# Optimization experiments

Measured on AMD Instinct MI355X. Metric: run time of the kernel, lower is better.

## Reference

```python
import jax, jax.numpy as jnp
import numpy as np

N_NODES = 50000
N_EDGES = 800000
IN_CH = 512
HID = 256
HEADS = 8
OUT_CH = 64


def _glorot(key, shape):
    fan_in = shape[0] if len(shape) == 2 else shape[-1]
    return jax.random.normal(key, shape, jnp.float32) / jnp.sqrt(jnp.float32(fan_in))


def setup_inputs() -> dict:
    key = jax.random.key(0)
    ks = jax.random.split(key, 16)
    C = HID // HEADS  # 32, per-head dim
    return {
        "x": jax.random.normal(ks[0], (N_NODES, IN_CH), jnp.float32),
        "edge_index": jax.random.randint(ks[1], (2, N_EDGES), 0, N_NODES, jnp.int32),
        # layer 0: in -> heads*C, concat
        "W0": _glorot(ks[2], (IN_CH, HEADS * C)),
        "a_src0": _glorot(ks[3], (HEADS, C)),
        "a_dst0": _glorot(ks[4], (HEADS, C)),
        "b0": jnp.zeros((HEADS * C,), jnp.float32),
        # layer 1: hidden -> heads*C, concat
        "W1": _glorot(ks[5], (HID, HEADS * C)),
        "a_src1": _glorot(ks[6], (HEADS, C)),
        "a_dst1": _glorot(ks[7], (HEADS, C)),
        "b1": jnp.zeros((HEADS * C,), jnp.float32),
        # layer 2: hidden -> out_ch, 1 head, mean (concat=False)
        "W2": _glorot(ks[8], (HID, 1 * OUT_CH)),
        "a_src2": _glorot(ks[9], (1, OUT_CH)),
        "a_dst2": _glorot(ks[10], (1, OUT_CH)),
        "b2": jnp.zeros((OUT_CH,), jnp.float32),
    }


def gat_conv(x, W, a_src, a_dst, b, src, dst, concat):
    """PyG GATConv (self-loops already appended to src/dst), eval mode."""
    N = x.shape[0]
    H, C = a_src.shape
    h = (x @ W).reshape(N, H, C)                      # [N,H,C]
    alpha_src = jnp.sum(h * a_src, axis=-1)           # [N,H]
    alpha_dst = jnp.sum(h * a_dst, axis=-1)           # [N,H]
    e = jax.nn.leaky_relu(alpha_src[src] + alpha_dst[dst], 0.2)  # [E,H]
    # softmax over incoming edges per destination node
    m = jax.ops.segment_max(e, dst, num_segments=N)   # [N,H]
    m = jnp.where(jnp.isfinite(m), m, 0.0)
    w = jnp.exp(e - m[dst])
    s = jax.ops.segment_sum(w, dst, num_segments=N)
    alpha = w / (s[dst] + 1e-16)                      # [E,H]
    out = jax.ops.segment_sum(alpha[:, :, None] * h[src], dst, num_segments=N)
    out = out.reshape(N, H * C) if concat else out.mean(axis=1)
    return out + b


def reference(x, edge_index, W0, a_src0, a_dst0, b0, W1, a_src1, a_dst1, b1, W2, a_src2, a_dst2, b2):
    N = x.shape[0]
    loop = jnp.arange(N, dtype=edge_index.dtype)      # add_self_loops=True
    src = jnp.concatenate([edge_index[0], loop])
    dst = jnp.concatenate([edge_index[1], loop])
    # dropout is identity in eval mode
    h = jax.nn.elu(gat_conv(x, W0, a_src0, a_dst0, b0, src, dst, True))
    h = jax.nn.elu(gat_conv(h, W1, a_src1, a_dst1, b1, src, dst, True))
    h = gat_conv(h, W2, a_src2, a_dst2, b2, src, dst, False)
    return jax.nn.log_softmax(h, axis=1)
```

## Files before the change

kernel.cpp:

```cpp
#include <hip/hip_runtime.h>
#include <hip/hip_bf16.h>

typedef __attribute__((ext_vector_type(8))) short short8;
typedef __attribute__((ext_vector_type(4))) float f32x4;
typedef __attribute__((ext_vector_type(2))) float f32x2;
typedef __attribute__((ext_vector_type(4))) unsigned short us4;

__device__ __forceinline__ ushort f2bf(float f) {
    unsigned u = __float_as_uint(f);
    u += 0x7FFFu + ((u >> 16) & 1u);
    return (ushort)(u >> 16);
}
__device__ __forceinline__ float bf2f(ushort h) {
    return __uint_as_float(((unsigned)h) << 16);
}
__device__ __forceinline__ float lrelu(float e) { return (e >= 0.f) ? e : 0.2f * e; }
__device__ __forceinline__ unsigned char f2fp8(float v) {
    return (unsigned char)(__builtin_amdgcn_cvt_pk_fp8_f32(v, v, 0, false) & 0xFF);
}
__device__ __forceinline__ void gload16(const void* g, void* l) {
    __builtin_amdgcn_global_load_lds(
        (const __attribute__((address_space(1))) unsigned int*)g,
        (__attribute__((address_space(3))) unsigned int*)l, 16, 0, 0);
}
__device__ __forceinline__ short8 cvt8(f32x4 a, f32x4 b) {
    short8 v;
#pragma unroll
    for (int j = 0; j < 4; ++j) {
        v[j] = (short)f2bf(a[j]);
        v[4 + j] = (short)f2bf(b[j]);
    }
    return v;
}

__global__ void k_hist(const int* __restrict__ dst, int* __restrict__ deg, int e) {
    int i = blockIdx.x * blockDim.x + threadIdx.x;
    if (i < e) atomicAdd(&deg[dst[i]], 1);
}
__global__ void k_scanA(const int* __restrict__ deg, int* __restrict__ bsum, int n) {
    __shared__ int sd[256];
    int t = blockIdx.x * 256 + threadIdx.x;
    sd[threadIdx.x] = (t < n) ? deg[t] + 1 : 0;
    __syncthreads();
    for (int off = 128; off > 0; off >>= 1) {
        if (threadIdx.x < off) sd[threadIdx.x] += sd[threadIdx.x + off];
        __syncthreads();
    }
    if (threadIdx.x == 0) bsum[blockIdx.x] = sd[0];
}
__global__ void k_scanC(const int* __restrict__ deg, const int* __restrict__ bsum,
                        int* __restrict__ rowptr, int* __restrict__ cursor,
                        int n, int etot, int nb) {
    __shared__ int sb[256];
    __shared__ int sd[256];
    __shared__ int sbx[256];
    int i = threadIdx.x;
    int bv = (i < nb) ? bsum[i] : 0;
    sb[i] = bv;
    __syncthreads();
    for (int off = 1; off < 256; off <<= 1) {
        int tv = (i >= off) ? sb[i - off] : 0;
        __syncthreads();
        sb[i] += tv;
        __syncthreads();
    }
    sbx[i] = sb[i] - bv;
    __syncthreads();
    int boff = sbx[blockIdx.x];

    int t = blockIdx.x * 256 + i;
    int v = (t < n) ? deg[t] + 1 : 0;
    sd[i] = v;
    __syncthreads();
    for (int off = 1; off < 256; off <<= 1) {
        int tv = (i >= off) ? sd[i - off] : 0;
        __syncthreads();
        sd[i] += tv;
        __syncthreads();
    }
    if (t < n) {
        int ex = boff + sd[i] - v;
        rowptr[t] = ex;
        cursor[t] = ex;
        if (t == n - 1) rowptr[n] = etot;
    }
}
__global__ void k_scatter(const int* __restrict__ ei, int* __restrict__ cursor,
                          int* __restrict__ col, int e, int n) {
    int i = blockIdx.x * blockDim.x + threadIdx.x;
    int etot = e + n;
    if (i >= etot) return;
    int s, d;
    if (i < e) { s = ei[i]; d = ei[e + i]; }
    else       { s = i - e; d = s; }
    int pos = atomicAdd(&cursor[d], 1);
    col[pos] = s;
}

__global__ void k_wcvt3(const float* __restrict__ W0, ushort* __restrict__ T0,
                        const float* __restrict__ W1, ushort* __restrict__ T1,
                        const float* __restrict__ W2, ushort* __restrict__ T2,
                        int* __restrict__ deg, int n) {
    int i = blockIdx.x * blockDim.x + threadIdx.x;
    if (i < n) deg[i] = 0;
    if (i < 131072) {
        int k = i >> 8, c = i & 255;
        T0[(size_t)c * 512 + k] = f2bf(W0[i]);
    } else if (i < 196608) {
        int j = i - 131072;
        int k = j >> 8, c = j & 255;
        T1[(size_t)c * 256 + k] = f2bf(W1[j]);
    } else if (i < 212992) {
        int j = i - 196608;
        int k = j >> 6, c = j & 63;
        T2[(size_t)c * 256 + k] = f2bf(W2[j]);
    }
}

template <int K, bool AF32>
__global__ __launch_bounds__(256, 8) void k_gemm(const void* __restrict__ Ap,
                                                 const ushort* __restrict__ BT,
                                                 unsigned char* __restrict__ Cp,
                                                 const float* __restrict__ asv,
                                                 const float* __restrict__ adv,
                                                 float* __restrict__ asrc,
                                                 float* __restrict__ adst, int M) {
    constexpr int BM = 32, BK = 32, BN = 128;
    constexpr int NK = K / BK;
    constexpr int BU = BN * BK / 8;
    __shared__ __align__(16) ushort lds[2][BU * 8];

    const int t = threadIdx.x;
    const int wid = t >> 6, lane = t & 63;
    const int lr = lane & 15, lg = lane >> 4;
    const int wm = wid >> 1, wn = wid & 1;
    const int bm0 = blockIdx.x * BM;
    const int bn0 = blockIdx.y * BN;

    int arow = bm0 + wm * 16 + lr;
    if (arow >= M) arow = M - 1;

    int b_off[4];
#pragma unroll
    for (int nf = 0; nf < 4; ++nf) {
        int col = wn * 64 + nf * 16 + lr;
        b_off[nf] = col * 64 + ((lg ^ ((col >> 1) & 3)) << 4);
    }

    f32x4 acc[4];
#pragma unroll
    for (int nf = 0; nf < 4; ++nf) acc[nf] = f32x4{0.f, 0.f, 0.f, 0.f};

    f32x4 rn0, rn1;
    short8 aNext;

    auto stage_B = [&](int buf, int kk) {
#pragma unroll
        for (int i = 0; i < 2; ++i) {
            int u = t + i * 256;
            int col = u >> 2;
            int g = (u & 3) ^ ((col >> 1) & 3);
            const ushort* src = BT + (size_t)(bn0 + col) * K + kk + g * 8;
            gload16(src, &lds[buf][u * 8]);
        }
    };
    auto load_A = [&](int kk) {
        if constexpr (AF32) {
            const float* src = (const float*)Ap + (size_t)arow * K + kk + lg * 8;
            rn0 = *(const f32x4*)src;
            rn1 = *(const f32x4*)(src + 4);
        } else {
            aNext = *(const short8*)((const ushort*)Ap + (size_t)arow * K + kk + lg * 8);
        }
    };
    auto compute = [&](int buf, short8 af) {
        const char* base = (const char*)lds[buf];
        short8 bf_[4];
#pragma unroll
        for (int nf = 0; nf < 4; ++nf) bf_[nf] = *(const short8*)(base + b_off[nf]);
#pragma unroll
        for (int nf = 0; nf < 4; ++nf)
            acc[nf] = __builtin_amdgcn_mfma_f32_16x16x32_bf16(af, bf_[nf], acc[nf], 0, 0, 0);
    };

    load_A(0);
    stage_B(0, 0);
    __syncthreads();

    int buf = 0;
    for (int ks = 0; ks < NK; ++ks) {
        short8 aCur;
        if constexpr (AF32) aCur = cvt8(rn0, rn1);
        else aCur = aNext;
        if (ks + 1 < NK) {
            load_A((ks + 1) * BK);
            stage_B(buf ^ 1, (ks + 1) * BK);
        }
        compute(buf, aCur);
        __syncthreads();
        buf ^= 1;
    }

#pragma unroll
    for (int nf = 0; nf < 4; ++nf) {
        int col = bn0 + wn * 64 + nf * 16 + lr;
#pragma unroll
        for (int p = 0; p < 4; ++p) {
            int row = bm0 + wm * 16 + lg * 4 + p;
            if (row < M)
                Cp[(size_t)row * 256 + col] = f2fp8(acc[nf][p]);
        }
    }

    {
        float cs[4], cd[4];
#pragma unroll
        for (int nf = 0; nf < 4; ++nf) {
            int col = bn0 + wn * 64 + nf * 16 + lr;
            cs[nf] = asv[col];
            cd[nf] = adv[col];
        }
        const int hb = (bn0 >> 5) + wn * 2;
#pragma unroll
        for (int p = 0; p < 4; ++p) {
            float sA = acc[0][p] * cs[0] + acc[1][p] * cs[1];
            float sB = acc[2][p] * cs[2] + acc[3][p] * cs[3];
            float dA = acc[0][p] * cd[0] + acc[1][p] * cd[1];
            float dB = acc[2][p] * cd[2] + acc[3][p] * cd[3];
#pragma unroll
            for (int off = 1; off < 16; off <<= 1) {
                sA += __shfl_xor(sA, off);
                sB += __shfl_xor(sB, off);
                dA += __shfl_xor(dA, off);
                dB += __shfl_xor(dB, off);
            }
            int row = bm0 + wm * 16 + lg * 4 + p;
            if (lr == 0 && row < M) {
                asrc[row * 8 + hb] = sA;
                asrc[row * 8 + hb + 1] = sB;
                adst[row * 8 + hb] = dA;
                adst[row * 8 + hb + 1] = dB;
            }
        }
    }
}

__global__ __launch_bounds__(256) void k_gemm2(const ushort* __restrict__ Ap,
                                               const ushort* __restrict__ BT,
                                               ushort* __restrict__ Cp,
                                               const float* __restrict__ asv,
                                               const float* __restrict__ adv,
                                               float* __restrict__ asrc,
                                               float* __restrict__ adst, int M) {
    constexpr int K = 256, BM = 64, BK = 32;
    constexpr int NK = K / BK;
    constexpr int BU = 64 * BK / 8;
    __shared__ __align__(16) ushort lds[2][BU * 8];

    const int t = threadIdx.x;
    const int wid = t >> 6, lane = t & 63;
    const int lr = lane & 15, lg = lane >> 4;
    const int bm0 = blockIdx.x * BM;

    int arow = bm0 + wid * 16 + lr;
    if (arow >= M) arow = M - 1;

    int b_off[4];
#pragma unroll
    for (int nf = 0; nf < 4; ++nf) {
        int col = nf * 16 + lr;
        b_off[nf] = col * 64 + ((lg ^ ((col >> 1) & 3)) << 4);
    }

    f32x4 acc[4];
#pragma unroll
    for (int nf = 0; nf < 4; ++nf) acc[nf] = f32x4{0.f, 0.f, 0.f, 0.f};

    short8 aNext;
    auto stage_B = [&](int buf, int kk) {
        int u = t;
        int col = u >> 2;
        int g = (u & 3) ^ ((col >> 1) & 3);
        const ushort* src = BT + (size_t)col * K + kk + g * 8;
        gload16(src, &lds[buf][u * 8]);
    };
    auto load_A = [&](int kk) {
        aNext = *(const short8*)(Ap + (size_t)arow * K + kk + lg * 8);
    };
    auto compute = [&](int buf, short8 af) {
        const char* base = (const char*)lds[buf];
        short8 bf_[4];
#pragma unroll
        for (int nf = 0; nf < 4; ++nf) bf_[nf] = *(const short8*)(base + b_off[nf]);
#pragma unroll
        for (int nf = 0; nf < 4; ++nf)
            acc[nf] = __builtin_amdgcn_mfma_f32_16x16x32_bf16(af, bf_[nf], acc[nf], 0, 0, 0);
    };

    load_A(0);
    stage_B(0, 0);
    __syncthreads();
    int buf = 0;
    for (int ks = 0; ks < NK; ++ks) {
        short8 aCur = aNext;
        if (ks + 1 < NK) {
            load_A((ks + 1) * BK);
            stage_B(buf ^ 1, (ks + 1) * BK);
        }
        compute(buf, aCur);
        __syncthreads();
        buf ^= 1;
    }

    float cs[4], cd[4];
#pragma unroll
    for (int nf = 0; nf < 4; ++nf) {
        cs[nf] = asv[nf * 16 + lr];
        cd[nf] = adv[nf * 16 + lr];
    }
#pragma unroll
    for (int p = 0; p < 4; ++p) {
        int row = bm0 + wid * 16 + lg * 4 + p;
#pragma unroll
        for (int nf = 0; nf < 4; ++nf) {
            if (row < M)
                Cp[(size_t)row * 64 + nf * 16 + lr] = f2bf(acc[nf][p]);
        }
        float sA = acc[0][p] * cs[0] + acc[1][p] * cs[1] +
                   acc[2][p] * cs[2] + acc[3][p] * cs[3];
        float dA = acc[0][p] * cd[0] + acc[1][p] * cd[1] +
                   acc[2][p] * cd[2] + acc[3][p] * cd[3];
#pragma unroll
        for (int off = 1; off < 16; off <<= 1) {
            sA += __shfl_xor(sA, off);
            dA += __shfl_xor(dA, off);
        }
        if (lr == 0 && row < M) {
            asrc[row] = sA;
            adst[row] = dA;
        }
    }
}

#define MAXW 96
__global__ __launch_bounds__(128) void k_agg(const unsigned char* __restrict__ h8,
                                             const float* __restrict__ asrc,
                                             const float* __restrict__ adst,
                                             const int* __restrict__ rowptr,
                                             const int* __restrict__ col,
                                             const float* __restrict__ bias,
                                             ushort* __restrict__ anext, int n) {
    __shared__ float wl[2][MAXW * 8];
    int wid = threadIdx.x >> 6;
    int lane = threadIdx.x & 63;
    int node = blockIdx.x * 2 + wid;
    if (node >= n) return;
    int beg = rowptr[node], end = rowptr[node + 1];
    int deg = end - beg;
    int hd = lane >> 3;
    int eo = lane & 7;
    float ad = adst[node * 8 + hd];
    float* wp = wl[wid];

    float sacc = 0.f;
    for (int jb = eo; jb < deg; jb += 8) {
        int s = col[beg + jb];
        float w = __expf(lrelu(asrc[s * 8 + hd] + ad));
        if (jb < MAXW) wp[jb * 8 + hd] = w;
        sacc += w;
    }
    sacc += __shfl_xor(sacc, 1);
    sacc += __shfl_xor(sacc, 2);
    sacc += __shfl_xor(sacc, 4);
    float inv = 1.f / (sacc + 1e-16f);

    int nl = (deg < MAXW) ? deg : MAXW;
    float a0 = 0.f, a1 = 0.f, a2 = 0.f, a3 = 0.f;
    int jb = 0;
    for (; jb + 8 <= nl; jb += 8) {
        int sv[8];
#pragma unroll
        for (int i = 0; i < 8; ++i) sv[i] = col[beg + jb + i];
        unsigned gv[8];
#pragma unroll
        for (int i = 0; i < 8; ++i) gv[i] = *(const unsigned*)(h8 + (size_t)sv[i] * 256 + lane * 4);
        float wv[8];
#pragma unroll
        for (int i = 0; i < 8; ++i) wv[i] = wp[(jb + i) * 8 + hd];
#pragma unroll
        for (int i = 0; i < 8; ++i) {
            a0 += wv[i] * __builtin_amdgcn_cvt_f32_fp8(gv[i], 0);
            a1 += wv[i] * __builtin_amdgcn_cvt_f32_fp8(gv[i], 1);
            a2 += wv[i] * __builtin_amdgcn_cvt_f32_fp8(gv[i], 2);
            a3 += wv[i] * __builtin_amdgcn_cvt_f32_fp8(gv[i], 3);
        }
    }
    for (; jb < nl; ++jb) {
        int s = col[beg + jb];
        unsigned g = *(const unsigned*)(h8 + (size_t)s * 256 + lane * 4);
        float w = wp[jb * 8 + hd];
        a0 += w * __builtin_amdgcn_cvt_f32_fp8(g, 0);
        a1 += w * __builtin_amdgcn_cvt_f32_fp8(g, 1);
        a2 += w * __builtin_amdgcn_cvt_f32_fp8(g, 2);
        a3 += w * __builtin_amdgcn_cvt_f32_fp8(g, 3);
    }
    for (; jb < deg; ++jb) {
        int s = col[beg + jb];
        unsigned g = *(const unsigned*)(h8 + (size_t)s * 256 + lane * 4);
        float w = __expf(lrelu(asrc[s * 8 + hd] + ad));
        a0 += w * __builtin_amdgcn_cvt_f32_fp8(g, 0);
        a1 += w * __builtin_amdgcn_cvt_f32_fp8(g, 1);
        a2 += w * __builtin_amdgcn_cvt_f32_fp8(g, 2);
        a3 += w * __builtin_amdgcn_cvt_f32_fp8(g, 3);
    }
    f32x4 bv = *(const f32x4*)(bias + lane * 4);
    float v0 = a0 * inv + bv[0];
    float v1 = a1 * inv + bv[1];
    float v2 = a2 * inv + bv[2];
    float v3 = a3 * inv + bv[3];
    v0 = (v0 > 0.f) ? v0 : expm1f(v0);
    v1 = (v1 > 0.f) ? v1 : expm1f(v1);
    v2 = (v2 > 0.f) ? v2 : expm1f(v2);
    v3 = (v3 > 0.f) ? v3 : expm1f(v3);
    us4 o;
    o[0] = f2bf(v0); o[1] = f2bf(v1); o[2] = f2bf(v2); o[3] = f2bf(v3);
    *(us4*)(anext + (size_t)node * 256 + lane * 4) = o;
}

__global__ __launch_bounds__(128) void k_agg2(const ushort* __restrict__ h2,
                                              const float* __restrict__ asrc,
                                              const float* __restrict__ adst,
                                              const int* __restrict__ rowptr,
                                              const int* __restrict__ col,
                                              const float* __restrict__ bias,
                                              float* __restrict__ out, int n) {
    int wid = threadIdx.x >> 6;
    int lane = threadIdx.x & 63;
    int node = blockIdx.x * 2 + wid;
    if (node >= n) return;
    int beg = rowptr[node], end = rowptr[node + 1];
    int deg = end - beg;
    float ad = adst[node];
    int g = lane >> 3;
    int ch = (lane & 7) * 8;

    f32x2 acc2[4];
#pragma unroll
    for (int i = 0; i < 4; ++i) acc2[i] = f32x2{0.f, 0.f};
    float ssum = 0.f;
    for (int p = 0; p < deg; p += 8) {
        int jb = p + g;
        float w = 0.f;
        uint4 gv = {0u, 0u, 0u, 0u};
        if (jb < deg) {
            int s = col[beg + jb];
            gv = *(const uint4*)(h2 + (size_t)s * 64 + ch);
            w = __expf(lrelu(asrc[s] + ad));
        }
        ssum += w;
        f32x2 w2 = {w, w};
        f32x2 p0 = {__uint_as_float(gv.x << 16), __uint_as_float(gv.x & 0xFFFF0000u)};
        f32x2 p1 = {__uint_as_float(gv.y << 16), __uint_as_float(gv.y & 0xFFFF0000u)};
        f32x2 p2 = {__uint_as_float(gv.z << 16), __uint_as_float(gv.z & 0xFFFF0000u)};
        f32x2 p3 = {__uint_as_float(gv.w << 16), __uint_as_float(gv.w & 0xFFFF0000u)};
        acc2[0] += w2 * p0;
        acc2[1] += w2 * p1;
        acc2[2] += w2 * p2;
        acc2[3] += w2 * p3;
    }
    float v[8];
#pragma unroll
    for (int i = 0; i < 4; ++i) { v[2 * i] = acc2[i].x; v[2 * i + 1] = acc2[i].y; }
#pragma unroll
    for (int off = 8; off < 64; off <<= 1) {
        ssum += __shfl_xor(ssum, off);
#pragma unroll
        for (int i = 0; i < 8; ++i) v[i] += __shfl_xor(v[i], off);
    }
    float inv = 1.f / (ssum + 1e-16f);
#pragma unroll
    for (int i = 0; i < 8; ++i) v[i] = v[i] * inv + bias[ch + i];
    float mx = v[0];
#pragma unroll
    for (int i = 1; i < 8; ++i) mx = fmaxf(mx, v[i]);
    mx = fmaxf(mx, __shfl_xor(mx, 1));
    mx = fmaxf(mx, __shfl_xor(mx, 2));
    mx = fmaxf(mx, __shfl_xor(mx, 4));
    float se = 0.f;
#pragma unroll
    for (int i = 0; i < 8; ++i) se += __expf(v[i] - mx);
    se += __shfl_xor(se, 1);
    se += __shfl_xor(se, 2);
    se += __shfl_xor(se, 4);
    float ls = mx + logf(se);
    if (g == 0) {
        f32x4 o0, o1;
#pragma unroll
        for (int i = 0; i < 4; ++i) { o0[i] = v[i] - ls; o1[i] = v[4 + i] - ls; }
        *(f32x4*)(out + (size_t)node * 64 + ch) = o0;
        *(f32x4*)(out + (size_t)node * 64 + ch + 4) = o1;
    }
}

extern "C" void kernel_launch(void* const* d_in, const int* in_sizes, int n_in,
                              void* d_out, int out_size, void* d_ws, size_t ws_size,
                              hipStream_t stream) {
    const float* x   = (const float*)d_in[0];
    const int*   ei  = (const int*)d_in[1];
    const float* W0  = (const float*)d_in[2];
    const float* as0 = (const float*)d_in[3];
    const float* ad0 = (const float*)d_in[4];
    const float* b0  = (const float*)d_in[5];
    const float* W1  = (const float*)d_in[6];
    const float* as1 = (const float*)d_in[7];
    const float* ad1 = (const float*)d_in[8];
    const float* b1  = (const float*)d_in[9];
    const float* W2  = (const float*)d_in[10];
    const float* as2 = (const float*)d_in[11];
    const float* ad2 = (const float*)d_in[12];
    const float* b2  = (const float*)d_in[13];
    float* out = (float*)d_out;

    const int N = in_sizes[0] / 512;
    const int E = in_sizes[1] / 2;
    const int ETOT = E + N;

    char* ws = (char*)d_ws;
    size_t off = 0;
    auto alloc = [&](size_t bytes) -> void* {
        off = (off + 255) & ~(size_t)255;
        void* p = ws + off;
        off += bytes;
        return p;
    };
    int* rowptr = (int*)alloc((size_t)(N + 1) * 4);
    int* cursor = (int*)alloc((size_t)N * 4);
    int* deg    = (int*)alloc((size_t)N * 4);
    int* bsum   = (int*)alloc(1024);
    int* colb   = (int*)alloc((size_t)ETOT * 4);
    ushort* WT0 = (ushort*)alloc((size_t)256 * 512 * 2);
    ushort* WT1 = (ushort*)alloc((size_t)256 * 256 * 2);
    ushort* WT2 = (ushort*)alloc((size_t)64 * 256 * 2);
    unsigned char* h8 = (unsigned char*)alloc((size_t)N * 256);
    ushort* abf = (ushort*)alloc((size_t)N * 256 * 2);
    float* asrc = (float*)alloc((size_t)N * 8 * 4);
    float* adst = (float*)alloc((size_t)N * 8 * 4);
    ushort* h2   = (ushort*)h8;
    float* asrc2 = asrc;
    float* adst2 = adst;

    const int nblk = (N + 255) / 256;

    k_wcvt3<<<832, 256, 0, stream>>>(W0, WT0, W1, WT1, W2, WT2, deg, N);

    k_hist<<<(E + 255) / 256, 256, 0, stream>>>(ei + E, deg, E);
    k_scanA<<<nblk, 256, 0, stream>>>(deg, bsum, N);
    k_scanC<<<nblk, 256, 0, stream>>>(deg, bsum, rowptr, cursor, N, ETOT, nblk);
    k_scatter<<<(ETOT + 255) / 256, 256, 0, stream>>>(ei, cursor, colb, E, N);

    const dim3 g01((N + 31) / 32, 2);
    const int gblk = (N + 63) / 64;
    const int ablk = (N + 1) / 2;

    k_gemm<512, true><<<g01, 256, 0, stream>>>(x, WT0, h8, as0, ad0, asrc, adst, N);
    k_agg<<<ablk, 128, 0, stream>>>(h8, asrc, adst, rowptr, colb, b0, abf, N);

    k_gemm<256, false><<<g01, 256, 0, stream>>>(abf, WT1, h8, as1, ad1, asrc, adst, N);
    k_agg<<<ablk, 128, 0, stream>>>(h8, asrc, adst, rowptr, colb, b1, abf, N);

    k_gemm2<<<gblk, 256, 0, stream>>>(abf, WT2, h2, as2, ad2, asrc2, adst2, N);
    k_agg2<<<ablk, 128, 0, stream>>>(h2, asrc2, adst2, rowptr, colb, b2, out, N);
}
```

Measured before the change: 364.1 us.

## Stage full weight slab in LDS once and enlarge GEMM tiles to 1024-thread blocks

The GEMM kernels now load the whole B (weight) slice for all K into LDS once at kernel start, dropping the per-K-step double-buffer staging and the barrier inside the loop. Blocks grow to 1024 threads covering 256 (or 512) rows, and each wave computes two 16-row M fragments so each B fragment is reused twice. This aims to cut redundant weight traffic and sync overhead. In exchange it uses large LDS (128KB for K=512), which limits occupancy to one block per CU, and there is no overlap between the initial B load and compute.

```diff
diff --git a/kernel.cpp b/kernel.cpp
--- a/kernel.cpp
+++ b/kernel.cpp
@@ -118,27 +118,31 @@
 }
 
 template <int K, bool AF32>
-__global__ __launch_bounds__(256, 8) void k_gemm(const void* __restrict__ Ap,
-                                                 const ushort* __restrict__ BT,
-                                                 unsigned char* __restrict__ Cp,
-                                                 const float* __restrict__ asv,
-                                                 const float* __restrict__ adv,
-                                                 float* __restrict__ asrc,
-                                                 float* __restrict__ adst, int M) {
-    constexpr int BM = 32, BK = 32, BN = 128;
-    constexpr int NK = K / BK;
-    constexpr int BU = BN * BK / 8;
-    __shared__ __align__(16) ushort lds[2][BU * 8];
+__global__ __launch_bounds__(1024) void k_gemm(const void* __restrict__ Ap,
+                                               const ushort* __restrict__ BT,
+                                               unsigned char* __restrict__ Cp,
+                                               const float* __restrict__ asv,
+                                               const float* __restrict__ adv,
+                                               float* __restrict__ asrc,
+                                               float* __restrict__ adst, int M) {
+    constexpr int NK = K / 32;
+    constexpr int NU = K / 64;
+    __shared__ __align__(16) ushort lds[128 * K];
 
     const int t = threadIdx.x;
     const int wid = t >> 6, lane = t & 63;
     const int lr = lane & 15, lg = lane >> 4;
-    const int wm = wid >> 1, wn = wid & 1;
-    const int bm0 = blockIdx.x * BM;
-    const int bn0 = blockIdx.y * BN;
-
-    int arow = bm0 + wm * 16 + lr;
-    if (arow >= M) arow = M - 1;
+    const int rg = wid >> 1, wn = wid & 1;
+    const int bx = blockIdx.x >> 1;
+    const int bn0 = (blockIdx.x & 1) * 128;
+    const int bm0 = bx * 256;
+
+    int arow[2];
+#pragma unroll
+    for (int mf = 0; mf < 2; ++mf) {
+        int r = bm0 + rg * 32 + mf * 16 + lr;
+        arow[mf] = (r < M) ? r : M - 1;
+    }
 
     int b_off[4];
 #pragma unroll
@@ -147,68 +151,72 @@
         b_off[nf] = col * 64 + ((lg ^ ((col >> 1) & 3)) << 4);
     }
 
-    f32x4 acc[4];
-#pragma unroll
-    for (int nf = 0; nf < 4; ++nf) acc[nf] = f32x4{0.f, 0.f, 0.f, 0.f};
-
-    f32x4 rn0, rn1;
-    short8 aNext;
-
-    auto stage_B = [&](int buf, int kk) {
-#pragma unroll
-        for (int i = 0; i < 2; ++i) {
-            int u = t + i * 256;
-            int col = u >> 2;
-            int g = (u & 3) ^ ((col >> 1) & 3);
-            const ushort* src = BT + (size_t)(bn0 + col) * K + kk + g * 8;
-            gload16(src, &lds[buf][u * 8]);
+#pragma unroll
+    for (int i = 0; i < NU; ++i) {
+        int u = t + i * 1024;
+        int ks = u >> 9;
+        int v = u & 511;
+        int col = v >> 2;
+        int g = (v & 3) ^ ((col >> 1) & 3);
+        const ushort* src = BT + (size_t)(bn0 + col) * K + ks * 32 + g * 8;
+        gload16(src, &lds[u * 8]);
+    }
+
+    f32x4 acc[2][4];
+#pragma unroll
+    for (int mf = 0; mf < 2; ++mf)
+#pragma unroll
+        for (int nf = 0; nf < 4; ++nf) acc[mf][nf] = f32x4{0.f, 0.f, 0.f, 0.f};
+
+    f32x4 rn[2][2];
+    short8 aNext[2];
+
+    auto load_A = [&](int kk) {
+#pragma unroll
+        for (int mf = 0; mf < 2; ++mf) {
+            if constexpr (AF32) {
+                const float* src = (const float*)Ap + (size_t)arow[mf] * K + kk + lg * 8;
+                rn[mf][0] = *(const f32x4*)src;
+                rn[mf][1] = *(const f32x4*)(src + 4);
+            } else {
+                aNext[mf] = *(const short8*)((const ushort*)Ap + (size_t)arow[mf] * K + kk + lg * 8);
+            }
         }
     };
-    auto load_A = [&](int kk) {
-        if constexpr (AF32) {
-            const float* src = (const float*)Ap + (size_t)arow * K + kk + lg * 8;
-            rn0 = *(const f32x4*)src;
-            rn1 = *(const f32x4*)(src + 4);
-        } else {
-            aNext = *(const short8*)((const ushort*)Ap + (size_t)arow * K + kk + lg * 8);
-        }
-    };
-    auto compute = [&](int buf, short8 af) {
-        const char* base = (const char*)lds[buf];
+
+    load_A(0);
+    __syncthreads();
+
+    for (int ks = 0; ks < NK; ++ks) {
+        short8 aCur[2];
+#pragma unroll
+        for (int mf = 0; mf < 2; ++mf) {
+            if constexpr (AF32) aCur[mf] = cvt8(rn[mf][0], rn[mf][1]);
+            else aCur[mf] = aNext[mf];
+        }
+        if (ks + 1 < NK) load_A((ks + 1) * 32);
+        const char* base = (const char*)lds + ks * 8192;
         short8 bf_[4];
 #pragma unroll
         for (int nf = 0; nf < 4; ++nf) bf_[nf] = *(const short8*)(base + b_off[nf]);
 #pragma unroll
-        for (int nf = 0; nf < 4; ++nf)
-            acc[nf] = __builtin_amdgcn_mfma_f32_16x16x32_bf16(af, bf_[nf], acc[nf], 0, 0, 0);
-    };
-
-    load_A(0);
-    stage_B(0, 0);
-    __syncthreads();
-
-    int buf = 0;
-    for (int ks = 0; ks < NK; ++ks) {
-        short8 aCur;
-        if constexpr (AF32) aCur = cvt8(rn0, rn1);
-        else aCur = aNext;
-        if (ks + 1 < NK) {
-            load_A((ks + 1) * BK);
-            stage_B(buf ^ 1, (ks + 1) * BK);
-        }
-        compute(buf, aCur);
-        __syncthreads();
-        buf ^= 1;
-    }
-
-#pragma unroll
-    for (int nf = 0; nf < 4; ++nf) {
-        int col = bn0 + wn * 64 + nf * 16 + lr;
-#pragma unroll
-        for (int p = 0; p < 4; ++p) {
-            int row = bm0 + wm * 16 + lg * 4 + p;
-            if (row < M)
-                Cp[(size_t)row * 256 + col] = f2fp8(acc[nf][p]);
+        for (int mf = 0; mf < 2; ++mf)
+#pragma unroll
+            for (int nf = 0; nf < 4; ++nf)
+                acc[mf][nf] = __builtin_amdgcn_mfma_f32_16x16x32_bf16(aCur[mf], bf_[nf], acc[mf][nf], 0, 0, 0);
+    }
+
+#pragma unroll
+    for (int mf = 0; mf < 2; ++mf) {
+#pragma unroll
+        for (int nf = 0; nf < 4; ++nf) {
+            int col = bn0 + wn * 64 + nf * 16 + lr;
+#pragma unroll
+            for (int p = 0; p < 4; ++p) {
+                int row = bm0 + rg * 32 + mf * 16 + lg * 4 + p;
+                if (row < M)
+                    Cp[(size_t)row * 256 + col] = f2fp8(acc[mf][nf][p]);
+            }
         }
     }
 
@@ -222,48 +230,53 @@
         }
         const int hb = (bn0 >> 5) + wn * 2;
 #pragma unroll
-        for (int p = 0; p < 4; ++p) {
-            float sA = acc[0][p] * cs[0] + acc[1][p] * cs[1];
-            float sB = acc[2][p] * cs[2] + acc[3][p] * cs[3];
-            float dA = acc[0][p] * cd[0] + acc[1][p] * cd[1];
-            float dB = acc[2][p] * cd[2] + acc[3][p] * cd[3];
-#pragma unroll
-            for (int off = 1; off < 16; off <<= 1) {
-                sA += __shfl_xor(sA, off);
-                sB += __shfl_xor(sB, off);
-                dA += __shfl_xor(dA, off);
-                dB += __shfl_xor(dB, off);
+        for (int mf = 0; mf < 2; ++mf) {
+#pragma unroll
+            for (int p = 0; p < 4; ++p) {
+                float sA = acc[mf][0][p] * cs[0] + acc[mf][1][p] * cs[1];
+                float sB = acc[mf][2][p] * cs[2] + acc[mf][3][p] * cs[3];
+                float dA = acc[mf][0][p] * cd[0] + acc[mf][1][p] * cd[1];
+                float dB = acc[mf][2][p] * cd[2] + acc[mf][3][p] * cd[3];
+#pragma unroll
+                for (int off = 1; off < 16; off <<= 1) {
+                    sA += __shfl_xor(sA, off);
+                    sB += __shfl_xor(sB, off);
+                    dA += __shfl_xor(dA, off);
+                    dB += __shfl_xor(dB, off);
+                }
+                int row = bm0 + rg * 32 + mf * 16 + lg * 4 + p;
+                if (lr == 0 && row < M) {
+                    asrc[row * 8 + hb] = sA;
+                    asrc[row * 8 + hb + 1] = sB;
+                    adst[row * 8 + hb] = dA;
+                    adst[row * 8 + hb + 1] = dB;
+                }
             }
-            int row = bm0 + wm * 16 + lg * 4 + p;
-            if (lr == 0 && row < M) {
-                asrc[row * 8 + hb] = sA;
-                asrc[row * 8 + hb + 1] = sB;
-                adst[row * 8 + hb] = dA;
-                adst[row * 8 + hb + 1] = dB;
-            }
-        }
-    }
-}
-
-__global__ __launch_bounds__(256) void k_gemm2(const ushort* __restrict__ Ap,
-                                               const ushort* __restrict__ BT,
-                                               ushort* __restrict__ Cp,
-                                               const float* __restrict__ asv,
-                                               const float* __restrict__ adv,
-                                               float* __restrict__ asrc,
-                                               float* __restrict__ adst, int M) {
-    constexpr int K = 256, BM = 64, BK = 32;
-    constexpr int NK = K / BK;
-    constexpr int BU = 64 * BK / 8;
-    __shared__ __align__(16) ushort lds[2][BU * 8];
+        }
+    }
+}
+
+__global__ __launch_bounds__(1024) void k_gemm2(const ushort* __restrict__ Ap,
+                                                const ushort* __restrict__ BT,
+                                                ushort* __restrict__ Cp,
+                                                const float* __restrict__ asv,
+                                                const float* __restrict__ adv,
+                                                float* __restrict__ asrc,
+                                                float* __restrict__ adst, int M) {
+    constexpr int K = 256, NK = 8;
+    __shared__ __align__(16) ushort lds[64 * K];
 
     const int t = threadIdx.x;
     const int wid = t >> 6, lane = t & 63;
     const int lr = lane & 15, lg = lane >> 4;
-    const int bm0 = blockIdx.x * BM;
-
-    int arow = bm0 + wid * 16 + lr;
-    if (arow >= M) arow = M - 1;
+    const int bm0 = blockIdx.x * 512;
+
+    int arow[2];
+#pragma unroll
+    for (int mf = 0; mf < 2; ++mf) {
+        int r = bm0 + wid * 32 + mf * 16 + lr;
+        arow[mf] = (r < M) ? r : M - 1;
+    }
 
     int b_off[4];
 #pragma unroll
@@ -272,44 +285,45 @@
         b_off[nf] = col * 64 + ((lg ^ ((col >> 1) & 3)) << 4);
     }
 
-    f32x4 acc[4];
-#pragma unroll
-    for (int nf = 0; nf < 4; ++nf) acc[nf] = f32x4{0.f, 0.f, 0.f, 0.f};
-
-    short8 aNext;
-    auto stage_B = [&](int buf, int kk) {
-        int u = t;
-        int col = u >> 2;
-        int g = (u & 3) ^ ((col >> 1) & 3);
-        const ushort* src = BT + (size_t)col * K + kk + g * 8;
-        gload16(src, &lds[buf][u * 8]);
+#pragma unroll
+    for (int i = 0; i < 2; ++i) {
+        int u = t + i * 1024;
+        int ks = u >> 8;
+        int v = u & 255;
+        int col = v >> 2;
+        int g = (v & 3) ^ ((col >> 1) & 3);
+        const ushort* src = BT + (size_t)col * K + ks * 32 + g * 8;
+        gload16(src, &lds[u * 8]);
+    }
+
+    f32x4 acc[2][4];
+#pragma unroll
+    for (int mf = 0; mf < 2; ++mf)
+#pragma unroll
+        for (int nf = 0; nf < 4; ++nf) acc[mf][nf] = f32x4{0.f, 0.f, 0.f, 0.f};
+
+    short8 aNext[2];
+    auto load_A = [&](int kk) {
+#pragma unroll
+        for (int mf = 0; mf < 2; ++mf)
+            aNext[mf] = *(const short8*)(Ap + (size_t)arow[mf] * K + kk + lg * 8);
     };
-    auto load_A = [&](int kk) {
-        aNext = *(const short8*)(Ap + (size_t)arow * K + kk + lg * 8);
-    };
-    auto compute = [&](int buf, short8 af) {
-        const char* base = (const char*)lds[buf];
+
+    load_A(0);
+    __syncthreads();
+
+    for (int ks = 0; ks < NK; ++ks) {
+        short8 aCur[2] = {aNext[0], aNext[1]};
+        if (ks + 1 < NK) load_A((ks + 1) * 32);
+        const char* base = (const char*)lds + ks * 4096;
         short8 bf_[4];
 #pragma unroll
         for (int nf = 0; nf < 4; ++nf) bf_[nf] = *(const short8*)(base + b_off[nf]);
 #pragma unroll
-        for (int nf = 0; nf < 4; ++nf)
-            acc[nf] = __builtin_amdgcn_mfma_f32_16x16x32_bf16(af, bf_[nf], acc[nf], 0, 0, 0);
-    };
-
-    load_A(0);
-    stage_B(0, 0);
-    __syncthreads();
-    int buf = 0;
-    for (int ks = 0; ks < NK; ++ks) {
-        short8 aCur = aNext;
-        if (ks + 1 < NK) {
-            load_A((ks + 1) * BK);
-            stage_B(buf ^ 1, (ks + 1) * BK);
-        }
-        compute(buf, aCur);
-        __syncthreads();
-        buf ^= 1;
+        for (int mf = 0; mf < 2; ++mf)
+#pragma unroll
+            for (int nf = 0; nf < 4; ++nf)
+                acc[mf][nf] = __builtin_amdgcn_mfma_f32_16x16x32_bf16(aCur[mf], bf_[nf], acc[mf][nf], 0, 0, 0);
     }
 
     float cs[4], cd[4];
@@ -319,25 +333,28 @@
         cd[nf] = adv[nf * 16 + lr];
     }
 #pragma unroll
-    for (int p = 0; p < 4; ++p) {
-        int row = bm0 + wid * 16 + lg * 4 + p;
-#pragma unroll
-        for (int nf = 0; nf < 4; ++nf) {
-            if (row < M)
-                Cp[(size_t)row * 64 + nf * 16 + lr] = f2bf(acc[nf][p]);
-        }
-        float sA = acc[0][p] * cs[0] + acc[1][p] * cs[1] +
-                   acc[2][p] * cs[2] + acc[3][p] * cs[3];
-        float dA = acc[0][p] * cd[0] + acc[1][p] * cd[1] +
-                   acc[2][p] * cd[2] + acc[3][p] * cd[3];
-#pragma unroll
-        for (int off = 1; off < 16; off <<= 1) {
-            sA += __shfl_xor(sA, off);
-            dA += __shfl_xor(dA, off);
-        }
-        if (lr == 0 && row < M) {
-            asrc[row] = sA;
-            adst[row] = dA;
+    for (int mf = 0; mf < 2; ++mf) {
+#pragma unroll
+        for (int p = 0; p < 4; ++p) {
+            int row = bm0 + wid * 32 + mf * 16 + lg * 4 + p;
+#pragma unroll
+            for (int nf = 0; nf < 4; ++nf) {
+                if (row < M)
+                    Cp[(size_t)row * 64 + nf * 16 + lr] = f2bf(acc[mf][nf][p]);
+            }
+            float sA = acc[mf][0][p] * cs[0] + acc[mf][1][p] * cs[1] +
+                       acc[mf][2][p] * cs[2] + acc[mf][3][p] * cs[3];
+            float dA = acc[mf][0][p] * cd[0] + acc[mf][1][p] * cd[1] +
+                       acc[mf][2][p] * cd[2] + acc[mf][3][p] * cd[3];
+#pragma unroll
+            for (int off = 1; off < 16; off <<= 1) {
+                sA += __shfl_xor(sA, off);
+                dA += __shfl_xor(dA, off);
+            }
+            if (lr == 0 && row < M) {
+                asrc[row] = sA;
+                adst[row] = dA;
+            }
         }
     }
 }
@@ -558,16 +575,16 @@
     k_scanC<<<nblk, 256, 0, stream>>>(deg, bsum, rowptr, cursor, N, ETOT, nblk);
     k_scatter<<<(ETOT + 255) / 256, 256, 0, stream>>>(ei, cursor, colb, E, N);
 
-    const dim3 g01((N + 31) / 32, 2);
-    const int gblk = (N + 63) / 64;
+    const int g01 = 2 * ((N + 255) / 256);
+    const int g2  = (N + 511) / 512;
     const int ablk = (N + 1) / 2;
 
-    k_gemm<512, true><<<g01, 256, 0, stream>>>(x, WT0, h8, as0, ad0, asrc, adst, N);
+    k_gemm<512, true><<<g01, 1024, 0, stream>>>(x, WT0, h8, as0, ad0, asrc, adst, N);
     k_agg<<<ablk, 128, 0, stream>>>(h8, asrc, adst, rowptr, colb, b0, abf, N);
 
-    k_gemm<256, false><<<g01, 256, 0, stream>>>(abf, WT1, h8, as1, ad1, asrc, adst, N);
+    k_gemm<256, false><<<g01, 1024, 0, stream>>>(abf, WT1, h8, as1, ad1, asrc, adst, N);
     k_agg<<<ablk, 128, 0, stream>>>(h8, asrc, adst, rowptr, colb, b1, abf, N);
 
-    k_gemm2<<<gblk, 256, 0, stream>>>(abf, WT2, h2, as2, ad2, asrc2, adst2, N);
+    k_gemm2<<<g2, 1024, 0, stream>>>(abf, WT2, h2, as2, ad2, asrc2, adst2, N);
     k_agg2<<<ablk, 128, 0, stream>>>(h2, asrc2, adst2, rowptr, colb, b2, out, N);
 }
```

Measured after the change: 371.5 us. +2.0%, slower.
